# Kernel tuning notes

Measured on AMD Instinct MI355X. Metric: run time of the kernel, lower is better.

Reference implementation:

```python
import jax, jax.numpy as jnp
import numpy as np

N_NODES = 40000
N_EDGES = 640000
D_FEAT = 128


def setup_inputs() -> dict:
    key = jax.random.key(0)
    k1, k2, k3 = jax.random.split(key, 3)
    feats = jax.random.normal(k1, (N_NODES, D_FEAT), dtype=jnp.float32)
    src = jax.random.randint(k2, (N_EDGES,), 0, N_NODES, dtype=jnp.int32)
    dst = jax.random.randint(k3, (N_EDGES,), 0, N_NODES, dtype=jnp.int32)
    return {"feats": feats, "src": src, "dst": dst}


def reference(feats, src, dst):
    n = feats.shape[0]
    # gather node features to edges and take L1 diff: u_sub_v then sum(|.|)
    diff = feats[src] - feats[dst]                                # [E, D]
    e = jnp.exp(-0.01 * jnp.sum(jnp.abs(diff), axis=-1))          # [E], exp(-1/100 * L1)
    # edge softmax grouped by destination node (numerically stable)
    m = jax.ops.segment_max(e, dst, num_segments=n)               # [N]
    ex = jnp.exp(e - m[dst])                                      # [E]
    s = jax.ops.segment_sum(ex, dst, num_segments=n)              # [N]
    out = ex / s[dst]                                             # [E]
    return out[:, None]                                           # [E, 1] (matches feats.view(-1,1,D) head dim)
```

## Files before the change

kernel.cpp:

```cpp
#include <hip/hip_runtime.h>
#include <math.h>

#define D_FEAT 128

__device__ __forceinline__ unsigned int bf16_rne(float x) {
    unsigned int u = __float_as_uint(x);
    return (u + 0x7fffu + ((u >> 16) & 1u)) >> 16;
}

__device__ __forceinline__ float l1_pair(unsigned int ua, unsigned int ub) {
    float a0 = __uint_as_float(ua << 16);
    float a1 = __uint_as_float(ua & 0xffff0000u);
    float b0 = __uint_as_float(ub << 16);
    float b1 = __uint_as_float(ub & 0xffff0000u);
    return fabsf(a0 - b0) + fabsf(a1 - b1);
}

__global__ __launch_bounds__(256) void prep_kernel(
    const float* __restrict__ feats, unsigned int* __restrict__ fb,
    float* __restrict__ s, int n_nodes, int n_vec)
{
    int i = blockIdx.x * blockDim.x + threadIdx.x;
    if (i < n_nodes) s[i] = 0.0f;
    if (i < n_vec) {
        const float4* fp = (const float4*)feats;
        float4 a = fp[2 * i];
        float4 b = fp[2 * i + 1];
        uint4 o;
        o.x = bf16_rne(a.x) | (bf16_rne(a.y) << 16);
        o.y = bf16_rne(a.z) | (bf16_rne(a.w) << 16);
        o.z = bf16_rne(b.x) | (bf16_rne(b.y) << 16);
        o.w = bf16_rne(b.z) | (bf16_rne(b.w) << 16);
        ((uint4*)fb)[i] = o;
    }
}

__global__ __launch_bounds__(256) void edge_kernel(
    const unsigned int* __restrict__ fb, const int* __restrict__ src,
    const int* __restrict__ dst, float* __restrict__ out,
    float* __restrict__ s, int n_edges)
{
    int tid  = blockIdx.x * blockDim.x + threadIdx.x;
    int l    = tid & 15;
    int edge = tid >> 4;
    if (edge >= n_edges) return;

    int srow = src[edge];
    int drow = dst[edge];
    const uint4* sp = (const uint4*)(fb + (size_t)srow * (D_FEAT / 2));
    const uint4* dp = (const uint4*)(fb + (size_t)drow * (D_FEAT / 2));
    uint4 a = sp[l];
    uint4 b = dp[l];
    float partial = l1_pair(a.x, b.x) + l1_pair(a.y, b.y)
                  + l1_pair(a.z, b.z) + l1_pair(a.w, b.w);
    #pragma unroll
    for (int mask = 8; mask >= 1; mask >>= 1)
        partial += __shfl_xor(partial, mask);

    if (l == 0) {
        float e = expf(-0.01f * partial);
        float w = expf(e);
        out[edge] = w;
        atomicAdd(s + drow, w);
    }
}

__global__ void norm_kernel(const int* __restrict__ dst, const float* __restrict__ s,
                            float* __restrict__ out, int n_edges)
{
    int i = blockIdx.x * blockDim.x + threadIdx.x;
    if (i >= n_edges) return;
    out[i] = out[i] / s[dst[i]];
}

extern "C" void kernel_launch(void* const* d_in, const int* in_sizes, int n_in,
                              void* d_out, int out_size, void* d_ws, size_t ws_size,
                              hipStream_t stream) {
    const float* feats = (const float*)d_in[0];
    const int*   src   = (const int*)d_in[1];
    const int*   dst   = (const int*)d_in[2];
    float* out = (float*)d_out;

    int n_edges = in_sizes[1];
    int n_nodes = in_sizes[0] / D_FEAT;
    int n_vec   = n_nodes * (D_FEAT / 8);

    float* s = (float*)d_ws;
    unsigned int* fb = (unsigned int*)((char*)d_ws + (size_t)n_nodes * sizeof(float));

    prep_kernel<<<(n_vec + 255) / 256, 256, 0, stream>>>(feats, fb, s, n_nodes, n_vec);

    int n_blocks_edge = (int)(((size_t)n_edges * 16 + 255) / 256);
    edge_kernel<<<n_blocks_edge, 256, 0, stream>>>(fb, src, dst, out, s, n_edges);

    norm_kernel<<<(n_edges + 255) / 256, 256, 0, stream>>>(dst, s, out, n_edges);
}
```

Measured before the change: 116.6 us.

## Switch gathered features to fp16 with packed dot and two edges per thread group

Features are now stored as fp16 instead of bf16, and the L1 distance uses packed half2 subtraction, a sign mask and fdot2 accumulation in place of scalar unpacking. Each group of 8 threads now handles two edges, with each thread loading two uint4 chunks per row. This cuts thread count and shuffle steps and puts more loads in flight per thread. The cost is more register pressure, and fp16 has a narrower range and different rounding than bf16, though normal-distributed inputs stay well within it.

```diff
diff --git a/kernel.cpp b/kernel.cpp
--- a/kernel.cpp
+++ b/kernel.cpp
@@ -1,23 +1,36 @@
 #include <hip/hip_runtime.h>
+#include <hip/hip_fp16.h>
 #include <math.h>
 
 #define D_FEAT 128
 
-__device__ __forceinline__ unsigned int bf16_rne(float x) {
-    unsigned int u = __float_as_uint(x);
-    return (u + 0x7fffu + ((u >> 16) & 1u)) >> 16;
+typedef _Float16 half2_t __attribute__((ext_vector_type(2)));
+
+__device__ __forceinline__ float l1_u(unsigned int ua, unsigned int ub, float acc) {
+    half2_t a = __builtin_bit_cast(half2_t, ua);
+    half2_t b = __builtin_bit_cast(half2_t, ub);
+    half2_t d = a - b;
+    unsigned int du = __builtin_bit_cast(unsigned int, d) & 0x7fff7fffu;
+    half2_t ad = __builtin_bit_cast(half2_t, du);
+    const half2_t one = {(_Float16)1.0f, (_Float16)1.0f};
+    return __builtin_amdgcn_fdot2(ad, one, acc, false);
 }
 
-__device__ __forceinline__ float l1_pair(unsigned int ua, unsigned int ub) {
-    float a0 = __uint_as_float(ua << 16);
-    float a1 = __uint_as_float(ua & 0xffff0000u);
-    float b0 = __uint_as_float(ub << 16);
-    float b1 = __uint_as_float(ub & 0xffff0000u);
-    return fabsf(a0 - b0) + fabsf(a1 - b1);
+__device__ __forceinline__ float l1_u4(uint4 a, uint4 b, float acc) {
+    acc = l1_u(a.x, b.x, acc);
+    acc = l1_u(a.y, b.y, acc);
+    acc = l1_u(a.z, b.z, acc);
+    acc = l1_u(a.w, b.w, acc);
+    return acc;
+}
+
+__device__ __forceinline__ unsigned int pkh(float x, float y) {
+    __half2 h = __halves2half2(__float2half_rn(x), __float2half_rn(y));
+    return __builtin_bit_cast(unsigned int, h);
 }
 
 __global__ __launch_bounds__(256) void prep_kernel(
-    const float* __restrict__ feats, unsigned int* __restrict__ fb,
+    const float* __restrict__ feats, unsigned int* __restrict__ fh,
     float* __restrict__ s, int n_nodes, int n_vec)
 {
     int i = blockIdx.x * blockDim.x + threadIdx.x;
@@ -27,41 +40,62 @@
         float4 a = fp[2 * i];
         float4 b = fp[2 * i + 1];
         uint4 o;
-        o.x = bf16_rne(a.x) | (bf16_rne(a.y) << 16);
-        o.y = bf16_rne(a.z) | (bf16_rne(a.w) << 16);
-        o.z = bf16_rne(b.x) | (bf16_rne(b.y) << 16);
-        o.w = bf16_rne(b.z) | (bf16_rne(b.w) << 16);
-        ((uint4*)fb)[i] = o;
+        o.x = pkh(a.x, a.y);
+        o.y = pkh(a.z, a.w);
+        o.z = pkh(b.x, b.y);
+        o.w = pkh(b.z, b.w);
+        ((uint4*)fh)[i] = o;
     }
 }
 
 __global__ __launch_bounds__(256) void edge_kernel(
-    const unsigned int* __restrict__ fb, const int* __restrict__ src,
+    const unsigned int* __restrict__ fh, const int* __restrict__ src,
     const int* __restrict__ dst, float* __restrict__ out,
     float* __restrict__ s, int n_edges)
 {
-    int tid  = blockIdx.x * blockDim.x + threadIdx.x;
-    int l    = tid & 15;
-    int edge = tid >> 4;
-    if (edge >= n_edges) return;
+    int tid = blockIdx.x * blockDim.x + threadIdx.x;
+    int l   = tid & 7;
+    int g   = tid >> 3;
+    int e0  = g * 2;
+    int e1  = e0 + 1;
+    if (e0 >= n_edges) return;
+    bool have1 = (e1 < n_edges);
 
-    int srow = src[edge];
-    int drow = dst[edge];
-    const uint4* sp = (const uint4*)(fb + (size_t)srow * (D_FEAT / 2));
-    const uint4* dp = (const uint4*)(fb + (size_t)drow * (D_FEAT / 2));
-    uint4 a = sp[l];
-    uint4 b = dp[l];
-    float partial = l1_pair(a.x, b.x) + l1_pair(a.y, b.y)
-                  + l1_pair(a.z, b.z) + l1_pair(a.w, b.w);
+    int s0 = src[e0], d0 = dst[e0];
+    int s1 = have1 ? src[e1] : s0;
+    int d1 = have1 ? dst[e1] : d0;
+
+    const uint4* t = (const uint4*)fh;
+    uint4 sa0 = t[(size_t)s0 * 16 + l];
+    uint4 sb0 = t[(size_t)s0 * 16 + l + 8];
+    uint4 da0 = t[(size_t)d0 * 16 + l];
+    uint4 db0 = t[(size_t)d0 * 16 + l + 8];
+    uint4 sa1 = t[(size_t)s1 * 16 + l];
+    uint4 sb1 = t[(size_t)s1 * 16 + l + 8];
+    uint4 da1 = t[(size_t)d1 * 16 + l];
+    uint4 db1 = t[(size_t)d1 * 16 + l + 8];
+
+    float p0 = 0.0f, p1 = 0.0f;
+    p0 = l1_u4(sa0, da0, p0);
+    p0 = l1_u4(sb0, db0, p0);
+    p1 = l1_u4(sa1, da1, p1);
+    p1 = l1_u4(sb1, db1, p1);
+
     #pragma unroll
-    for (int mask = 8; mask >= 1; mask >>= 1)
-        partial += __shfl_xor(partial, mask);
+    for (int mask = 4; mask >= 1; mask >>= 1) {
+        p0 += __shfl_xor(p0, mask);
+        p1 += __shfl_xor(p1, mask);
+    }
 
     if (l == 0) {
-        float e = expf(-0.01f * partial);
-        float w = expf(e);
-        out[edge] = w;
-        atomicAdd(s + drow, w);
+        float w0 = expf(expf(-0.01f * p0));
+        out[e0] = w0;
+        atomicAdd(s + d0, w0);
+        if (have1) {
+            float w1 = expf(expf(-0.01f * p1));
+            out[e1] = w1;
+            atomicAdd(s + d1, w1);
+        }
     }
 }
 
@@ -85,13 +119,14 @@
     int n_nodes = in_sizes[0] / D_FEAT;
     int n_vec   = n_nodes * (D_FEAT / 8);
 
-    float* s = (float*)d_ws;
-    unsigned int* fb = (unsigned int*)((char*)d_ws + (size_t)n_nodes * sizeof(float));
+    float* sseg = (float*)d_ws;
+    unsigned int* fh = (unsigned int*)((char*)d_ws + (size_t)n_nodes * sizeof(float));
 
-    prep_kernel<<<(n_vec + 255) / 256, 256, 0, stream>>>(feats, fb, s, n_nodes, n_vec);
+    prep_kernel<<<(n_vec + 255) / 256, 256, 0, stream>>>(feats, fh, sseg, n_nodes, n_vec);
 
-    int n_blocks_edge = (int)(((size_t)n_edges * 16 + 255) / 256);
-    edge_kernel<<<n_blocks_edge, 256, 0, stream>>>(fb, src, dst, out, s, n_edges);
+    long long threads = ((long long)n_edges + 1) / 2 * 8;
+    int n_blocks_edge = (int)((threads + 255) / 256);
+    edge_kernel<<<n_blocks_edge, 256, 0, stream>>>(fh, src, dst, out, sseg, n_edges);
 
-    norm_kernel<<<(n_edges + 255) / 256, 256, 0, stream>>>(dst, s, out, n_edges);
+    norm_kernel<<<(n_edges + 255) / 256, 256, 0, stream>>>(dst, sseg, out, n_edges);
 }
```

After: 116.9 us. Within noise of the previous version (+0.3%).
